# Kernel tuning notes

Measured on AMD Instinct MI355X. Metric: run time of the kernel, lower is better.

Reference implementation:

```python
import jax, jax.numpy as jnp
import numpy as np

N_NODES = 50000

def setup_inputs() -> dict:
    key = jax.random.key(0)
    k1, k2, k3, k4, k5, k6 = jax.random.split(key, 6)
    T, D, N, E = 10000, 128, N_NODES, 800000
    impact = jax.random.normal(k1, (T, D), dtype=jnp.float32)
    W = jax.random.normal(k2, (D, D), dtype=jnp.float32)
    M = jax.random.normal(k3, (D, D), dtype=jnp.float32)
    node_ids = jax.random.randint(k4, (N,), 0, T, dtype=jnp.int64)
    neighbor_ids = jax.random.randint(k5, (E,), 0, T, dtype=jnp.int64)
    neighbor_segments = jnp.sort(jax.random.randint(k6, (E,), 0, N, dtype=jnp.int64))
    return {"impact": impact, "W": W, "M": M, "node_ids": node_ids,
            "neighbor_ids": neighbor_ids, "neighbor_segments": neighbor_segments}

def reference(impact, W, M, node_ids, neighbor_ids, neighbor_segments):
    # Per node i (type k_i): s_i = relu(W @ h[k_i] + sum_{j in N(i)} M @ h[type_j])
    # result = softmax(sum_i s_i) over the D feature axis.
    self_feats = impact[node_ids]                          # (N, D) gather
    neigh_feats = impact[neighbor_ids]                     # (E, D) gather
    neigh_sum = jax.ops.segment_sum(neigh_feats, neighbor_segments,
                                    num_segments=N_NODES)  # (N, D) scatter-add
    pre = self_feats @ W.T + neigh_sum @ M.T               # (N, D)
    result = jnp.sum(jax.nn.relu(pre), axis=0)             # (D,)
    return jax.nn.softmax(result, axis=0)
```

## Files before the change

### kernel.cpp

```cpp
#include <hip/hip_runtime.h>

#define DDIM 128
#define ACC_BLOCKS 2048
#define NWALK (ACC_BLOCKS * 4)
#define RED_BLOCKS 64

typedef unsigned int uint;
typedef unsigned short ushort;

static __device__ __forceinline__ ushort f2bf(float x) {
    uint u = __float_as_uint(x);
    u += 0x7fffu + ((u >> 16) & 1u);
    return (ushort)(u >> 16);
}
static __device__ __forceinline__ float bflo(uint u) { return __uint_as_float(u << 16); }
static __device__ __forceinline__ float bfhi(uint u) { return __uint_as_float(u & 0xffff0000u); }

__global__ __launch_bounds__(256) void build_rowptr(
    const int* __restrict__ segs, int* __restrict__ rowptr, int N, int E)
{
    const int e = blockIdx.x * blockDim.x + threadIdx.x;
    if (e >= E) return;
    const int sc = segs[e];
    const int sp = (e == 0) ? -1 : segs[e - 1];
    for (int i = sp + 1; i <= sc; ++i) rowptr[i] = e;
    if (e == E - 1) {
        for (int i = sc + 1; i <= N; ++i) rowptr[i] = E;
    }
}

__global__ __launch_bounds__(256) void build_items(
    const int* __restrict__ segs,
    const int* __restrict__ rowptr,
    const int* __restrict__ node_ids,
    const int* __restrict__ neighbor_ids,
    int* __restrict__ items,
    int* __restrict__ wstart,
    int N, int E, int whoff, int mhoff)
{
    const int x = blockIdx.x * blockDim.x + threadIdx.x;
    const int K = N + E;
    if (x < E) {
        const int s = segs[x];
        const bool last = (x + 1 == E) || (segs[x + 1] != s);
        items[x + s + 1] = (mhoff + neighbor_ids[x] * 256) | (last ? (int)0x80000000 : 0);
    }
    if (x < N) {
        const int r = rowptr[x];
        const bool last = (rowptr[x + 1] == r);
        items[r + x] = (whoff + node_ids[x] * 256) | (last ? (int)0x80000000 : 0);
    }
    if (x <= NWALK) {
        const int t = (int)(((long long)x * K) / NWALK);
        int lo = 0, hi = N;
        while (lo < hi) {
            const int mid = (lo + hi) >> 1;
            if (rowptr[mid] + mid < t) lo = mid + 1; else hi = mid;
        }
        wstart[x] = rowptr[lo] + lo;
    }
    if (x == 0) {
#pragma unroll
        for (int q = 0; q < 8; ++q) items[K + q] = whoff;
    }
}

__global__ __launch_bounds__(128) void precompute_wh_mh(
    const float* __restrict__ impact,
    const float* __restrict__ W,
    const float* __restrict__ Mm,
    ushort* __restrict__ WhB,
    ushort* __restrict__ MhB,
    int T)
{
    const int d = threadIdx.x;
    const int row0 = blockIdx.x * 8;
    if (row0 >= T) return;
    const int rmax = min(8, T - row0);

    const float4* __restrict__ W4 = reinterpret_cast<const float4*>(W) + (size_t)d * 32;
    const float4* __restrict__ M4 = reinterpret_cast<const float4*>(Mm) + (size_t)d * 32;
    const float4* __restrict__ H4 = reinterpret_cast<const float4*>(impact);

    float accW[8], accM[8];
#pragma unroll
    for (int r = 0; r < 8; ++r) { accW[r] = 0.f; accM[r] = 0.f; }

    for (int kq = 0; kq < 32; ++kq) {
        const float4 wv = W4[kq];
        const float4 mv = M4[kq];
#pragma unroll
        for (int r = 0; r < 8; ++r) {
            const int rr = (r < rmax) ? (row0 + r) : (T - 1);
            const float4 hv = H4[(size_t)rr * 32 + kq];
            accW[r] = fmaf(hv.x, wv.x, accW[r]);
            accW[r] = fmaf(hv.y, wv.y, accW[r]);
            accW[r] = fmaf(hv.z, wv.z, accW[r]);
            accW[r] = fmaf(hv.w, wv.w, accW[r]);
            accM[r] = fmaf(hv.x, mv.x, accM[r]);
            accM[r] = fmaf(hv.y, mv.y, accM[r]);
            accM[r] = fmaf(hv.z, mv.z, accM[r]);
            accM[r] = fmaf(hv.w, mv.w, accM[r]);
        }
    }
    for (int r = 0; r < rmax; ++r) {
        WhB[(size_t)(row0 + r) * DDIM + d] = f2bf(accW[r]);
        MhB[(size_t)(row0 + r) * DDIM + d] = f2bf(accM[r]);
    }
}

__global__ __launch_bounds__(256, 8) void accumulate_items(
    const char* __restrict__ tab,
    const int* __restrict__ items,
    const int* __restrict__ wstart,
    float* __restrict__ partials)
{
    const int lane = threadIdx.x & 63;
    const int wv   = __builtin_amdgcn_readfirstlane(threadIdx.x >> 6);
    const int w    = blockIdx.x * 4 + wv;

    const uint lb = (uint)lane << 2;

    float c0 = 0.f, c1 = 0.f, a0 = 0.f, a1 = 0.f;

    int k    = __builtin_amdgcn_readfirstlane(wstart[w]);
    const int kend = __builtin_amdgcn_readfirstlane(wstart[w + 1]);

#define LDROW(IW) (*reinterpret_cast<const uint*>(tab + (((uint)(IW)) & 0x7fffffffu) + lb))
#define ACC(IW, V) { \
    c0 += bflo(V); c1 += bfhi(V); \
    if ((IW) < 0) { a0 += fmaxf(c0, 0.f); a1 += fmaxf(c1, 0.f); c0 = 0.f; c1 = 0.f; } }

    while (k < kend && (k & 7)) {
        const int iw = items[k];
        const uint v = LDROW(iw);
        ACC(iw, v);
        ++k;
    }
    while (k + 8 <= kend) {
        const int4 A = *reinterpret_cast<const int4*>(items + k);
        const int4 B = *reinterpret_cast<const int4*>(items + k + 4);
        const uint v0 = LDROW(A.x);
        const uint v1 = LDROW(A.y);
        const uint v2 = LDROW(A.z);
        const uint v3 = LDROW(A.w);
        const uint v4 = LDROW(B.x);
        const uint v5 = LDROW(B.y);
        const uint v6 = LDROW(B.z);
        const uint v7 = LDROW(B.w);
        ACC(A.x, v0); ACC(A.y, v1); ACC(A.z, v2); ACC(A.w, v3);
        ACC(B.x, v4); ACC(B.y, v5); ACC(B.z, v6); ACC(B.w, v7);
        k += 8;
    }
    while (k < kend) {
        const int iw = items[k];
        const uint v = LDROW(iw);
        ACC(iw, v);
        ++k;
    }

    a0 += fmaxf(c0, 0.f);
    a1 += fmaxf(c1, 0.f);

    __shared__ float red[4][DDIM];
    red[wv][lane * 2 + 0] = a0;
    red[wv][lane * 2 + 1] = a1;
    __syncthreads();
    const int tid = threadIdx.x;
    if (tid < DDIM) {
        partials[(size_t)blockIdx.x * DDIM + tid] =
            red[0][tid] + red[1][tid] + red[2][tid] + red[3][tid];
    }
}

__global__ __launch_bounds__(256) void reduce_partials(
    const float* __restrict__ partials, float* __restrict__ out2, int nb)
{
    const int d = threadIdx.x & (DDIM - 1);
    const int h = threadIdx.x >> 7;
    const int rows = nb / RED_BLOCKS;
    const int r0 = blockIdx.x * rows;
    float s = 0.f;
    for (int r = r0 + h; r < r0 + rows; r += 2)
        s += partials[(size_t)r * DDIM + d];
    __shared__ float red[2][DDIM];
    red[h][d] = s;
    __syncthreads();
    if (threadIdx.x < DDIM)
        out2[(size_t)blockIdx.x * DDIM + threadIdx.x] =
            red[0][threadIdx.x] + red[1][threadIdx.x];
}

__global__ __launch_bounds__(1024) void finalize_softmax(
    const float* __restrict__ p2, float* __restrict__ out, int nb)
{
    const int t = threadIdx.x;
    const int d = t & (DDIM - 1);
    const int g = t >> 7;

    float s = 0.f;
    for (int b = g; b < nb; b += 8)
        s += p2[(size_t)b * DDIM + d];

    __shared__ float red[8][DDIM];
    red[g][d] = s;
    __syncthreads();

    __shared__ float vec[DDIM];
    __shared__ float tmp[DDIM];
    if (g == 0) {
        float v = 0.f;
#pragma unroll
        for (int g2 = 0; g2 < 8; ++g2) v += red[g2][d];
        vec[d] = v;
    }
    __syncthreads();

    const float sv = vec[d];
    if (g == 0) tmp[d] = sv;
    __syncthreads();
    for (int off = 64; off > 0; off >>= 1) {
        if (t < off) tmp[t] = fmaxf(tmp[t], tmp[t + off]);
        __syncthreads();
    }
    const float mx = tmp[0];
    __syncthreads();
    const float ev = expf(sv - mx);
    if (g == 0) tmp[d] = ev;
    __syncthreads();
    for (int off = 64; off > 0; off >>= 1) {
        if (t < off) tmp[t] += tmp[t + off];
        __syncthreads();
    }
    if (g == 0) out[d] = ev / tmp[0];
}

extern "C" void kernel_launch(void* const* d_in, const int* in_sizes, int n_in,
                              void* d_out, int out_size, void* d_ws, size_t ws_size,
                              hipStream_t stream) {
    const float* impact        = (const float*)d_in[0];
    const float* W             = (const float*)d_in[1];
    const float* Mm            = (const float*)d_in[2];
    const int*   node_ids      = (const int*)d_in[3];
    const int*   neighbor_ids  = (const int*)d_in[4];
    const int*   neighbor_segs = (const int*)d_in[5];

    const int T = in_sizes[0] / DDIM;
    const int N = in_sizes[3];
    const int E = in_sizes[4];
    const int K = N + E;

    char* ws = (char*)d_ws;
    size_t off = 0;
    const int whoff = (int)off;
    ushort* WhB = (ushort*)(ws + off);  off += (size_t)T * DDIM * sizeof(ushort);
    const int mhoff = (int)off;
    ushort* MhB = (ushort*)(ws + off);  off += (size_t)T * DDIM * sizeof(ushort);
    float* partials = (float*)(ws + off); off += (size_t)ACC_BLOCKS * DDIM * sizeof(float);
    float* part2    = (float*)(ws + off); off += (size_t)RED_BLOCKS * DDIM * sizeof(float);
    int*   rowptr   = (int*)(ws + off);   off += (size_t)(N + 1) * sizeof(int);
    off = (off + 255) & ~(size_t)255;
    int*   items    = (int*)(ws + off);   off += (size_t)(K + 8) * sizeof(int);
    int*   wstart   = (int*)(ws + off);   off += (size_t)(NWALK + 1) * sizeof(int);
    float* outf     = (float*)d_out;

    build_rowptr<<<(E + 255) / 256, 256, 0, stream>>>(neighbor_segs, rowptr, N, E);
    build_items<<<(max(E, N) + 255) / 256, 256, 0, stream>>>(
        neighbor_segs, rowptr, node_ids, neighbor_ids, items, wstart, N, E, whoff, mhoff);
    precompute_wh_mh<<<(T + 7) / 8, 128, 0, stream>>>(impact, W, Mm, WhB, MhB, T);
    accumulate_items<<<ACC_BLOCKS, 256, 0, stream>>>(ws, items, wstart, partials);
    reduce_partials<<<RED_BLOCKS, 256, 0, stream>>>(partials, part2, ACC_BLOCKS);
    finalize_softmax<<<1, 1024, 0, stream>>>(part2, outf, RED_BLOCKS);
}
```

Before: 68.08 us.

## Use MFMA bf16 for table precompute, unroll gather by 16, fuse final reduce

```diff
diff --git a/kernel.cpp b/kernel.cpp
--- a/kernel.cpp
+++ b/kernel.cpp
@@ -7,6 +7,8 @@
 
 typedef unsigned int uint;
 typedef unsigned short ushort;
+typedef __attribute__((ext_vector_type(8))) short bf16x8;
+typedef __attribute__((ext_vector_type(4))) float f32x4;
 
 static __device__ __forceinline__ ushort f2bf(float x) {
     uint u = __float_as_uint(x);
@@ -17,9 +19,11 @@
 static __device__ __forceinline__ float bfhi(uint u) { return __uint_as_float(u & 0xffff0000u); }
 
 __global__ __launch_bounds__(256) void build_rowptr(
-    const int* __restrict__ segs, int* __restrict__ rowptr, int N, int E)
+    const int* __restrict__ segs, int* __restrict__ rowptr, int* __restrict__ done,
+    int N, int E)
 {
     const int e = blockIdx.x * blockDim.x + threadIdx.x;
+    if (e == 0) *done = 0;
     if (e >= E) return;
     const int sc = segs[e];
     const int sp = (e == 0) ? -1 : segs[e - 1];
@@ -61,11 +65,22 @@
     }
     if (x == 0) {
 #pragma unroll
-        for (int q = 0; q < 8; ++q) items[K + q] = whoff;
-    }
-}
-
-__global__ __launch_bounds__(128) void precompute_wh_mh(
+        for (int q = 0; q < 16; ++q) items[K + q] = whoff;
+    }
+}
+
+static __device__ __forceinline__ bf16x8 load_frag8(const float* base) {
+    const float4 p = *reinterpret_cast<const float4*>(base);
+    const float4 q = *reinterpret_cast<const float4*>(base + 4);
+    bf16x8 f;
+    f[0] = (short)f2bf(p.x); f[1] = (short)f2bf(p.y);
+    f[2] = (short)f2bf(p.z); f[3] = (short)f2bf(p.w);
+    f[4] = (short)f2bf(q.x); f[5] = (short)f2bf(q.y);
+    f[6] = (short)f2bf(q.z); f[7] = (short)f2bf(q.w);
+    return f;
+}
+
+__global__ __launch_bounds__(256) void precompute_mfma(
     const float* __restrict__ impact,
     const float* __restrict__ W,
     const float* __restrict__ Mm,
@@ -73,39 +88,48 @@
     ushort* __restrict__ MhB,
     int T)
 {
-    const int d = threadIdx.x;
-    const int row0 = blockIdx.x * 8;
-    if (row0 >= T) return;
-    const int rmax = min(8, T - row0);
-
-    const float4* __restrict__ W4 = reinterpret_cast<const float4*>(W) + (size_t)d * 32;
-    const float4* __restrict__ M4 = reinterpret_cast<const float4*>(Mm) + (size_t)d * 32;
-    const float4* __restrict__ H4 = reinterpret_cast<const float4*>(impact);
-
-    float accW[8], accM[8];
-#pragma unroll
-    for (int r = 0; r < 8; ++r) { accW[r] = 0.f; accM[r] = 0.f; }
-
-    for (int kq = 0; kq < 32; ++kq) {
-        const float4 wv = W4[kq];
-        const float4 mv = M4[kq];
-#pragma unroll
-        for (int r = 0; r < 8; ++r) {
-            const int rr = (r < rmax) ? (row0 + r) : (T - 1);
-            const float4 hv = H4[(size_t)rr * 32 + kq];
-            accW[r] = fmaf(hv.x, wv.x, accW[r]);
-            accW[r] = fmaf(hv.y, wv.y, accW[r]);
-            accW[r] = fmaf(hv.z, wv.z, accW[r]);
-            accW[r] = fmaf(hv.w, wv.w, accW[r]);
-            accM[r] = fmaf(hv.x, mv.x, accM[r]);
-            accM[r] = fmaf(hv.y, mv.y, accM[r]);
-            accM[r] = fmaf(hv.z, mv.z, accM[r]);
-            accM[r] = fmaf(hv.w, mv.w, accM[r]);
+    const int lane = threadIdx.x & 63;
+    const int wv   = threadIdx.x >> 6;
+    const int t0   = blockIdx.x * 32;
+    const int r16  = lane & 15;
+    const int kg   = lane >> 4;
+
+    bf16x8 A[2][4];
+#pragma unroll
+    for (int rt = 0; rt < 2; ++rt) {
+        int t = t0 + rt * 16 + r16;
+        if (t >= T) t = T - 1;
+        const float* abase = impact + (size_t)t * DDIM + kg * 8;
+#pragma unroll
+        for (int k0i = 0; k0i < 4; ++k0i)
+            A[rt][k0i] = load_frag8(abase + k0i * 32);
+    }
+
+#pragma unroll
+    for (int dti = 0; dti < 2; ++dti) {
+        const int d0 = (wv * 2 + dti) * 16;
+#pragma unroll
+        for (int m = 0; m < 2; ++m) {
+            const float* mat = (m == 0) ? W : Mm;
+            ushort* out = (m == 0) ? WhB : MhB;
+            const float* bbase = mat + (size_t)(d0 + r16) * DDIM + kg * 8;
+            f32x4 acc0 = {0.f, 0.f, 0.f, 0.f};
+            f32x4 acc1 = {0.f, 0.f, 0.f, 0.f};
+#pragma unroll
+            for (int k0i = 0; k0i < 4; ++k0i) {
+                const bf16x8 b = load_frag8(bbase + k0i * 32);
+                acc0 = __builtin_amdgcn_mfma_f32_16x16x32_bf16(A[0][k0i], b, acc0, 0, 0, 0);
+                acc1 = __builtin_amdgcn_mfma_f32_16x16x32_bf16(A[1][k0i], b, acc1, 0, 0, 0);
+            }
+            const int dcol = d0 + r16;
+#pragma unroll
+            for (int r = 0; r < 4; ++r) {
+                const int tr0 = t0 + kg * 4 + r;
+                const int tr1 = tr0 + 16;
+                if (tr0 < T) out[(size_t)tr0 * DDIM + dcol] = f2bf(acc0[r]);
+                if (tr1 < T) out[(size_t)tr1 * DDIM + dcol] = f2bf(acc1[r]);
+            }
         }
-    }
-    for (int r = 0; r < rmax; ++r) {
-        WhB[(size_t)(row0 + r) * DDIM + d] = f2bf(accW[r]);
-        MhB[(size_t)(row0 + r) * DDIM + d] = f2bf(accM[r]);
     }
 }
 
@@ -123,7 +147,7 @@
 
     float c0 = 0.f, c1 = 0.f, a0 = 0.f, a1 = 0.f;
 
-    int k    = __builtin_amdgcn_readfirstlane(wstart[w]);
+    int k = __builtin_amdgcn_readfirstlane(wstart[w]);
     const int kend = __builtin_amdgcn_readfirstlane(wstart[w + 1]);
 
 #define LDROW(IW) (*reinterpret_cast<const uint*>(tab + (((uint)(IW)) & 0x7fffffffu) + lb))
@@ -131,26 +155,37 @@
     c0 += bflo(V); c1 += bfhi(V); \
     if ((IW) < 0) { a0 += fmaxf(c0, 0.f); a1 += fmaxf(c1, 0.f); c0 = 0.f; c1 = 0.f; } }
 
-    while (k < kend && (k & 7)) {
+    while (k < kend && (k & 3)) {
         const int iw = items[k];
         const uint v = LDROW(iw);
         ACC(iw, v);
         ++k;
     }
-    while (k + 8 <= kend) {
-        const int4 A = *reinterpret_cast<const int4*>(items + k);
-        const int4 B = *reinterpret_cast<const int4*>(items + k + 4);
-        const uint v0 = LDROW(A.x);
-        const uint v1 = LDROW(A.y);
-        const uint v2 = LDROW(A.z);
-        const uint v3 = LDROW(A.w);
-        const uint v4 = LDROW(B.x);
-        const uint v5 = LDROW(B.y);
-        const uint v6 = LDROW(B.z);
-        const uint v7 = LDROW(B.w);
-        ACC(A.x, v0); ACC(A.y, v1); ACC(A.z, v2); ACC(A.w, v3);
-        ACC(B.x, v4); ACC(B.y, v5); ACC(B.z, v6); ACC(B.w, v7);
-        k += 8;
+    while (k + 16 <= kend) {
+        const int4 Ia = *reinterpret_cast<const int4*>(items + k);
+        const int4 Ib = *reinterpret_cast<const int4*>(items + k + 4);
+        const int4 Ic = *reinterpret_cast<const int4*>(items + k + 8);
+        const int4 Id = *reinterpret_cast<const int4*>(items + k + 12);
+        const uint v0  = LDROW(Ia.x); const uint v1  = LDROW(Ia.y);
+        const uint v2  = LDROW(Ia.z); const uint v3  = LDROW(Ia.w);
+        const uint v4  = LDROW(Ib.x); const uint v5  = LDROW(Ib.y);
+        const uint v6  = LDROW(Ib.z); const uint v7  = LDROW(Ib.w);
+        const uint v8  = LDROW(Ic.x); const uint v9  = LDROW(Ic.y);
+        const uint v10 = LDROW(Ic.z); const uint v11 = LDROW(Ic.w);
+        const uint v12 = LDROW(Id.x); const uint v13 = LDROW(Id.y);
+        const uint v14 = LDROW(Id.z); const uint v15 = LDROW(Id.w);
+        ACC(Ia.x, v0);  ACC(Ia.y, v1);  ACC(Ia.z, v2);  ACC(Ia.w, v3);
+        ACC(Ib.x, v4);  ACC(Ib.y, v5);  ACC(Ib.z, v6);  ACC(Ib.w, v7);
+        ACC(Ic.x, v8);  ACC(Ic.y, v9);  ACC(Ic.z, v10); ACC(Ic.w, v11);
+        ACC(Id.x, v12); ACC(Id.y, v13); ACC(Id.z, v14); ACC(Id.w, v15);
+        k += 16;
+    }
+    while (k + 4 <= kend) {
+        const int4 Ia = *reinterpret_cast<const int4*>(items + k);
+        const uint v0 = LDROW(Ia.x); const uint v1 = LDROW(Ia.y);
+        const uint v2 = LDROW(Ia.z); const uint v3 = LDROW(Ia.w);
+        ACC(Ia.x, v0); ACC(Ia.y, v1); ACC(Ia.z, v2); ACC(Ia.w, v3);
+        k += 4;
     }
     while (k < kend) {
         const int iw = items[k];
@@ -173,66 +208,60 @@
     }
 }
 
-__global__ __launch_bounds__(256) void reduce_partials(
-    const float* __restrict__ partials, float* __restrict__ out2, int nb)
-{
-    const int d = threadIdx.x & (DDIM - 1);
-    const int h = threadIdx.x >> 7;
-    const int rows = nb / RED_BLOCKS;
-    const int r0 = blockIdx.x * rows;
+__global__ __launch_bounds__(256) void reduce_softmax(
+    const float* __restrict__ partials, float* __restrict__ out2,
+    float* __restrict__ out, int* __restrict__ done, int nb)
+{
+    const int tid = threadIdx.x;
+    const int d = tid & (DDIM - 1);
+    const int h = tid >> 7;
+    {
+        const int rows = nb / RED_BLOCKS;
+        const int r0 = blockIdx.x * rows;
+        float s = 0.f;
+        for (int r = r0 + h; r < r0 + rows; r += 2)
+            s += partials[(size_t)r * DDIM + d];
+        __shared__ float red[2][DDIM];
+        red[h][d] = s;
+        __syncthreads();
+        if (tid < DDIM)
+            out2[(size_t)blockIdx.x * DDIM + tid] = red[0][tid] + red[1][tid];
+    }
+    __threadfence();
+    __shared__ int isLast;
+    if (tid == 0) {
+        const int v = atomicAdd(done, 1);
+        isLast = (v == RED_BLOCKS - 1) ? 1 : 0;
+    }
+    __syncthreads();
+    if (!isLast) return;
+    __threadfence();
+
     float s = 0.f;
-    for (int r = r0 + h; r < r0 + rows; r += 2)
-        s += partials[(size_t)r * DDIM + d];
-    __shared__ float red[2][DDIM];
-    red[h][d] = s;
-    __syncthreads();
-    if (threadIdx.x < DDIM)
-        out2[(size_t)blockIdx.x * DDIM + threadIdx.x] =
-            red[0][threadIdx.x] + red[1][threadIdx.x];
-}
-
-__global__ __launch_bounds__(1024) void finalize_softmax(
-    const float* __restrict__ p2, float* __restrict__ out, int nb)
-{
-    const int t = threadIdx.x;
-    const int d = t & (DDIM - 1);
-    const int g = t >> 7;
-
-    float s = 0.f;
-    for (int b = g; b < nb; b += 8)
-        s += p2[(size_t)b * DDIM + d];
-
-    __shared__ float red[8][DDIM];
-    red[g][d] = s;
+    for (int b = h; b < RED_BLOCKS; b += 2)
+        s += out2[(size_t)b * DDIM + d];
+    __shared__ float r2[2][DDIM];
+    r2[h][d] = s;
     __syncthreads();
 
     __shared__ float vec[DDIM];
     __shared__ float tmp[DDIM];
-    if (g == 0) {
-        float v = 0.f;
-#pragma unroll
-        for (int g2 = 0; g2 < 8; ++g2) v += red[g2][d];
-        vec[d] = v;
-    }
-    __syncthreads();
-
-    const float sv = vec[d];
-    if (g == 0) tmp[d] = sv;
-    __syncthreads();
-    for (int off = 64; off > 0; off >>= 1) {
-        if (t < off) tmp[t] = fmaxf(tmp[t], tmp[t + off]);
+    if (tid < DDIM) { vec[tid] = r2[0][tid] + r2[1][tid]; tmp[tid] = r2[0][tid] + r2[1][tid]; }
+    __syncthreads();
+    for (int o = 64; o > 0; o >>= 1) {
+        if (tid < o) tmp[tid] = fmaxf(tmp[tid], tmp[tid + o]);
         __syncthreads();
     }
     const float mx = tmp[0];
     __syncthreads();
-    const float ev = expf(sv - mx);
-    if (g == 0) tmp[d] = ev;
-    __syncthreads();
-    for (int off = 64; off > 0; off >>= 1) {
-        if (t < off) tmp[t] += tmp[t + off];
+    float ev = 0.f;
+    if (tid < DDIM) { ev = expf(vec[tid] - mx); tmp[tid] = ev; }
+    __syncthreads();
+    for (int o = 64; o > 0; o >>= 1) {
+        if (tid < o) tmp[tid] += tmp[tid + o];
         __syncthreads();
     }
-    if (g == 0) out[d] = ev / tmp[0];
+    if (tid < DDIM) out[tid] = ev / tmp[0];
 }
 
 extern "C" void kernel_launch(void* const* d_in, const int* in_sizes, int n_in,
@@ -259,16 +288,16 @@
     float* partials = (float*)(ws + off); off += (size_t)ACC_BLOCKS * DDIM * sizeof(float);
     float* part2    = (float*)(ws + off); off += (size_t)RED_BLOCKS * DDIM * sizeof(float);
     int*   rowptr   = (int*)(ws + off);   off += (size_t)(N + 1) * sizeof(int);
+    int*   done     = (int*)(ws + off);   off += 256;
     off = (off + 255) & ~(size_t)255;
-    int*   items    = (int*)(ws + off);   off += (size_t)(K + 8) * sizeof(int);
+    int*   items    = (int*)(ws + off);   off += (size_t)(K + 16) * sizeof(int);
     int*   wstart   = (int*)(ws + off);   off += (size_t)(NWALK + 1) * sizeof(int);
     float* outf     = (float*)d_out;
 
-    build_rowptr<<<(E + 255) / 256, 256, 0, stream>>>(neighbor_segs, rowptr, N, E);
+    build_rowptr<<<(E + 255) / 256, 256, 0, stream>>>(neighbor_segs, rowptr, done, N, E);
     build_items<<<(max(E, N) + 255) / 256, 256, 0, stream>>>(
         neighbor_segs, rowptr, node_ids, neighbor_ids, items, wstart, N, E, whoff, mhoff);
-    precompute_wh_mh<<<(T + 7) / 8, 128, 0, stream>>>(impact, W, Mm, WhB, MhB, T);
+    precompute_mfma<<<(T + 31) / 32, 256, 0, stream>>>(impact, W, Mm, WhB, MhB, T);
     accumulate_items<<<ACC_BLOCKS, 256, 0, stream>>>(ws, items, wstart, partials);
-    reduce_partials<<<RED_BLOCKS, 256, 0, stream>>>(partials, part2, ACC_BLOCKS);
-    finalize_softmax<<<1, 1024, 0, stream>>>(part2, outf, RED_BLOCKS);
-}
+    reduce_softmax<<<RED_BLOCKS, 256, 0, stream>>>(partials, part2, outf, done, ACC_BLOCKS);
+}
```

Result: faster. 66.04 us (-3.0%).
